# Optimization experiments

Measured on AMD Instinct MI355X. Metric: run time of the kernel, lower is better.

Reference implementation:

```python
import jax, jax.numpy as jnp
import numpy as np

NEG_SLOPE = 0.2


def gat_conv(h, src, dst, n_dst, W_src, W_dst, attn_l, attn_r, bias):
    # h: [N_src, F_in]; edges src->dst; dst nodes are a prefix of src nodes.
    H, D = attn_l.shape
    z_src = (h @ W_src).reshape(h.shape[0], H, D)          # [N_src, H, D]
    z_dst = (h[:n_dst] @ W_dst).reshape(n_dst, H, D)       # [N_dst, H, D]
    el = jnp.einsum('nhd,hd->nh', z_src, attn_l)           # [N_src, H]
    er = jnp.einsum('nhd,hd->nh', z_dst, attn_r)           # [N_dst, H]
    e = jax.nn.leaky_relu(el[src] + er[dst], NEG_SLOPE)    # [E, H]
    # numerically stable edge softmax over incoming edges of each dst node
    m = jax.ops.segment_max(e, dst, num_segments=n_dst)    # [N_dst, H]
    w = jnp.exp(e - m[dst])                                # [E, H]
    s = jax.ops.segment_sum(w, dst, num_segments=n_dst)    # [N_dst, H]
    alpha = w / s[dst]                                     # [E, H]
    msg = alpha[:, :, None] * z_src[src]                   # [E, H, D]
    out = jax.ops.segment_sum(msg, dst, num_segments=n_dst)
    return out + bias                                      # [N_dst, H, D]


def setup_inputs() -> dict:
    key = jax.random.key(0)
    ks = jax.random.split(key, 16)
    IN, HID, HEADS, NCLS = 256, 64, 4, 47
    N_SRC0, N_DST0, E0 = 200000, 50000, 500000
    N_DST1, E1 = 10000, 100000
    sc0 = 0.1
    inp = {
        'x': jax.random.normal(ks[0], (N_SRC0, IN), jnp.float32),
        'src0': jax.random.randint(ks[1], (E0,), 0, N_SRC0, jnp.int32),
        'dst0': jax.random.randint(ks[2], (E0,), 0, N_DST0, jnp.int32),
        'src1': jax.random.randint(ks[3], (E1,), 0, N_DST0, jnp.int32),
        'dst1': jax.random.randint(ks[4], (E1,), 0, N_DST1, jnp.int32),
        'num_dst0': N_DST0,
        'num_dst1': N_DST1,
        'W0_src': jax.random.normal(ks[5], (IN, HEADS * HID), jnp.float32) * sc0,
        'W0_dst': jax.random.normal(ks[6], (IN, HEADS * HID), jnp.float32) * sc0,
        'attn_l0': jax.random.normal(ks[7], (HEADS, HID), jnp.float32) * sc0,
        'attn_r0': jax.random.normal(ks[8], (HEADS, HID), jnp.float32) * sc0,
        'bias0': jnp.zeros((HEADS, HID), jnp.float32),
        'W1_src': jax.random.normal(ks[9], (HEADS * HID, HEADS * NCLS), jnp.float32) * sc0,
        'W1_dst': jax.random.normal(ks[10], (HEADS * HID, HEADS * NCLS), jnp.float32) * sc0,
        'attn_l1': jax.random.normal(ks[11], (HEADS, NCLS), jnp.float32) * sc0,
        'attn_r1': jax.random.normal(ks[12], (HEADS, NCLS), jnp.float32) * sc0,
        'bias1': jnp.zeros((HEADS, NCLS), jnp.float32),
    }
    return inp


def reference(x, src0, dst0, src1, dst1, num_dst0, num_dst1,
              W0_src, W0_dst, attn_l0, attn_r0, bias0,
              W1_src, W1_dst, attn_l1, attn_r1, bias1):
    # layer 0: GATConv + relu activation, flatten heads
    h = gat_conv(x, src0, dst0, num_dst0, W0_src, W0_dst, attn_l0, attn_r0, bias0)
    h = jax.nn.relu(h).reshape(num_dst0, -1)               # [N_dst0, H*HID]
    # layer 1: GATConv, no activation
    h = gat_conv(h, src1, dst1, num_dst1, W1_src, W1_dst, attn_l1, attn_r1, bias1)
    h = h.mean(axis=1)                                     # mean over heads -> [N_dst1, n_classes]
    return jax.nn.log_softmax(h, axis=-1)
```

## Files before the change

### kernel.cpp

```cpp
#include <hip/hip_runtime.h>
#include <math.h>

typedef _Float16 half8 __attribute__((ext_vector_type(8)));
typedef _Float16 half4 __attribute__((ext_vector_type(4)));
typedef float f32x16 __attribute__((ext_vector_type(16)));

constexpr int IN    = 256;
constexpr int NCLS  = 47;
constexpr int HD1   = 188;
constexpr float NEG_SLOPE = 0.2f;
constexpr int ND0 = 50000, ND1 = 10000;

static __device__ __forceinline__ float leaky(float x) {
    return x >= 0.f ? x : NEG_SLOPE * x;
}

__device__ __forceinline__ void gload16(const void* g, void* l) {
    __builtin_amdgcn_global_load_lds((const __attribute__((address_space(1))) void*)g,
                                     (__attribute__((address_space(3))) void*)l, 16, 0, 0);
}

__global__ __launch_bounds__(256) void prep_k(
        const float* __restrict__ W0s, const float* __restrict__ W1s,
        const float* __restrict__ W0d, const float* __restrict__ W1d,
        const float* __restrict__ ar0, const float* __restrict__ ar1,
        const float* __restrict__ b0,
        _Float16* __restrict__ B0t, _Float16* __restrict__ B1t,
        float* __restrict__ vr0T, float* __restrict__ vr1T, float* __restrict__ biasP) {
    int b = blockIdx.x, t = threadIdx.x;
    if (b < 256) {
        int id = b * 256 + t;
        int n = id >> 8, k = id & 255;
        B0t[n * 256 + k] = (_Float16)W0s[(size_t)k * 256 + n];
    } else if (b < 448) {
        int id = (b - 256) * 256 + t;
        int n = id >> 8, kpc = id & 255;
        int c = ((kpc & 7) << 5) | (kpc >> 3);
        B1t[n * 256 + kpc] = (n < HD1) ? (_Float16)W1s[(size_t)c * HD1 + n] : (_Float16)0.f;
    } else if (b == 448) {
        for (int i = t; i < 1024; i += 256) {
            int h = i >> 8, k = i & 255;
            float s = 0.f;
            for (int d = 0; d < 64; ++d) s += W0d[(size_t)k * 256 + h * 64 + d] * ar0[h * 64 + d];
            vr0T[h * 256 + k] = s;
        }
    } else if (b == 449) {
        for (int i = t; i < 1024; i += 256) {
            int h = i >> 8, kpc = i & 255;
            int c = ((kpc & 7) << 5) | (kpc >> 3);
            float s = 0.f;
            for (int d = 0; d < NCLS; ++d) s += W1d[(size_t)c * HD1 + h * NCLS + d] * ar1[h * NCLS + d];
            vr1T[h * 256 + kpc] = s;
        }
    } else {
        int c = ((t & 7) << 5) | (t >> 3);
        biasP[t] = b0[c];
    }
}

template <bool AHALF, int BCOLS, int NOUT, bool ZPC, int FEL>
__global__ __launch_bounds__(512, 2) void gemm32(const void* __restrict__ Av,
        const _Float16* __restrict__ Bt, void* __restrict__ Z,
        const float* __restrict__ attn_flat, float* __restrict__ el, int M, int ntiles) {
    constexpr int NCB  = BCOLS / 32;
    constexpr int ABUF = AHALF ? 1024 : 2048;
    __shared__ __align__(16) _Float16 Bs[BCOLS * 256];
    __shared__ __align__(16) char As[8 * 2 * ABUF];
    const int t = threadIdx.x, l = t & 63, w = t >> 6;
    const int l31 = l & 31, hi = l >> 5;
    const int G = gridDim.x;
    char* Areg = As + w * 2 * ABUF;

    constexpr int BITERS = (BCOLS * 32) / 512;
#pragma unroll
    for (int it = 0; it < BITERS; ++it) {
        int c = it * 512 + t;
        int col = c >> 5, sK = c & 31;
        int sKs = sK ^ (col & 7);
        gload16(Bt + (size_t)col * 256 + sKs * 8, (char*)Bs + (it * 512 + w * 64) * 16);
    }

    auto stageA = [&](int buf, int tile, int kst) {
        int base = tile * 256 + w * 32;
        if constexpr (AHALF) {
            int r = l >> 1, sl = l & 1;
            int row = base + r; if (row >= M) row = M - 1;
            int ks = sl ^ (r & 1);
            gload16((const _Float16*)Av + (size_t)row * 256 + kst * 16 + ks * 8,
                    Areg + buf * ABUF);
        } else {
#pragma unroll
            for (int i = 0; i < 2; ++i) {
                int c = i * 64 + l;
                int r = c >> 2, sl = c & 3;
                int row = base + r; if (row >= M) row = M - 1;
                int ks = sl ^ ((r >> 1) & 3);
                gload16((const float*)Av + (size_t)row * 256 + kst * 16 + ks * 4,
                        Areg + buf * ABUF + i * 1024);
            }
        }
    };

    int tile0 = blockIdx.x;
    stageA(0, tile0, 0);
    __syncthreads();

    float alv[NCB];
    int hs[NCB];
    if constexpr (FEL > 0) {
#pragma unroll
        for (int cb = 0; cb < NCB; ++cb) {
            int c = cb * 32 + l31;
            if constexpr (FEL == 1) { alv[cb] = attn_flat[c]; hs[cb] = cb >> 1; }
            else { alv[cb] = (c < NOUT) ? attn_flat[c] : 0.f;
                   hs[cb] = c < 47 ? 0 : c < 94 ? 1 : c < 141 ? 2 : 3; }
        }
    }

    int buf = 0;
    for (int tile = tile0; tile < ntiles; tile += G) {
        f32x16 acc[NCB];
#pragma unroll
        for (int cb = 0; cb < NCB; ++cb)
#pragma unroll
            for (int e = 0; e < 16; ++e) acc[cb][e] = 0.f;

#pragma unroll
        for (int kst = 0; kst < 16; ++kst) {
            if (kst < 15) {
                stageA(buf ^ 1, tile, kst + 1);
                if constexpr (AHALF) asm volatile("s_waitcnt vmcnt(1)" ::: "memory");
                else                 asm volatile("s_waitcnt vmcnt(2)" ::: "memory");
            } else if (tile + G < ntiles) {
                stageA(buf ^ 1, tile + G, 0);
                if constexpr (AHALF) asm volatile("s_waitcnt vmcnt(1)" ::: "memory");
                else                 asm volatile("s_waitcnt vmcnt(2)" ::: "memory");
            } else {
                asm volatile("s_waitcnt vmcnt(0)" ::: "memory");
            }
            half8 af;
            if constexpr (AHALF) {
                af = *(const half8*)(Areg + buf * ABUF + l31 * 32 + ((hi ^ (l31 & 1)) << 4));
            } else {
                const char* ab = Areg + buf * ABUF + l31 * 64;
                float4 f0 = *(const float4*)(ab + ((( 2 * hi)     ^ ((l31 >> 1) & 3)) << 4));
                float4 f1 = *(const float4*)(ab + (((2 * hi + 1) ^ ((l31 >> 1) & 3)) << 4));
                af[0] = (_Float16)f0.x; af[1] = (_Float16)f0.y;
                af[2] = (_Float16)f0.z; af[3] = (_Float16)f0.w;
                af[4] = (_Float16)f1.x; af[5] = (_Float16)f1.y;
                af[6] = (_Float16)f1.z; af[7] = (_Float16)f1.w;
            }
#pragma unroll
            for (int cb = 0; cb < NCB; ++cb) {
                half8 bf = *(const half8*)&Bs[(cb * 32 + l31) * 256 +
                                              (((kst * 2 + hi) ^ (l & 7)) << 3)];
                acc[cb] = __builtin_amdgcn_mfma_f32_32x32x16_f16(af, bf, acc[cb], 0, 0, 0);
            }
            buf ^= 1;
        }

        const int R0 = tile * 256 + w * 32;
#pragma unroll
        for (int q = 0; q < 16; ++q) {
            int row = (q & 3) + 8 * (q >> 2) + 4 * hi;
            int grow = R0 + row;
            if constexpr (ZPC) {
                half8 hv;
#pragma unroll
                for (int cb = 0; cb < NCB; ++cb) hv[cb] = (_Float16)acc[cb][q];
                if (grow < M)
                    *(half8*)((_Float16*)Z + (size_t)grow * 256 + l31 * 8) = hv;
            } else {
                if (grow < M) {
#pragma unroll
                    for (int cb = 0; cb < NCB; ++cb) {
                        int col = cb * 32 + l31;
                        if (col < NOUT)
                            ((float*)Z)[(size_t)grow * NOUT + col] = acc[cb][q];
                    }
                }
            }
            if constexpr (FEL > 0) {
                float sh0 = 0.f, sh1 = 0.f, sh2 = 0.f, sh3 = 0.f;
#pragma unroll
                for (int cb = 0; cb < NCB; ++cb) {
                    float v = acc[cb][q] * alv[cb];
                    sh0 += (hs[cb] == 0) ? v : 0.f;
                    sh1 += (hs[cb] == 1) ? v : 0.f;
                    sh2 += (hs[cb] == 2) ? v : 0.f;
                    sh3 += (hs[cb] == 3) ? v : 0.f;
                }
#pragma unroll
                for (int off = 1; off <= 16; off <<= 1) {
                    sh0 += __shfl_xor(sh0, off); sh1 += __shfl_xor(sh1, off);
                    sh2 += __shfl_xor(sh2, off); sh3 += __shfl_xor(sh3, off);
                }
                if (l31 == 0 && grow < M)
                    *(float4*)(el + (size_t)grow * 4) = make_float4(sh0, sh1, sh2, sh3);
            }
        }
    }
}

__global__ __launch_bounds__(256) void gemv_er_f32(const float* __restrict__ A,
        const float* __restrict__ vrT, float* __restrict__ er, int M) {
    int wv = threadIdx.x >> 6, lane = threadIdx.x & 63;
    int row = blockIdx.x * 4 + wv;
    if (row >= M) return;
    float4 xa = *(const float4*)(A + (size_t)row * IN + lane * 4);
    float s[4];
#pragma unroll
    for (int h = 0; h < 4; ++h) {
        float4 v = *(const float4*)(vrT + h * IN + lane * 4);
        s[h] = xa.x * v.x + xa.y * v.y + xa.z * v.z + xa.w * v.w;
    }
#pragma unroll
    for (int off = 32; off; off >>= 1)
#pragma unroll
        for (int h = 0; h < 4; ++h) s[h] += __shfl_xor(s[h], off);
    if (lane == 0) *(float4*)(er + (size_t)row * 4) = make_float4(s[0], s[1], s[2], s[3]);
}

__global__ __launch_bounds__(256) void gemv_er_f16(const _Float16* __restrict__ A,
        const float* __restrict__ vrT, float* __restrict__ er, int M) {
    int wv = threadIdx.x >> 6, lane = threadIdx.x & 63;
    int row = blockIdx.x * 4 + wv;
    if (row >= M) return;
    half4 ah = *(const half4*)(A + (size_t)row * IN + lane * 4);
    float a0 = (float)ah[0], a1 = (float)ah[1], a2 = (float)ah[2], a3 = (float)ah[3];
    float s[4];
#pragma unroll
    for (int h = 0; h < 4; ++h) {
        float4 v = *(const float4*)(vrT + h * IN + lane * 4);
        s[h] = a0 * v.x + a1 * v.y + a2 * v.z + a3 * v.w;
    }
#pragma unroll
    for (int off = 32; off; off >>= 1)
#pragma unroll
        for (int h = 0; h < 4; ++h) s[h] += __shfl_xor(s[h], off);
    if (lane == 0) *(float4*)(er + (size_t)row * 4) = make_float4(s[0], s[1], s[2], s[3]);
}

__global__ void hist2_k(const int* __restrict__ dst0, int E0,
                        const int* __restrict__ dst1, int E1, int* __restrict__ counts) {
    int i = blockIdx.x * blockDim.x + threadIdx.x;
    if (i < E0) atomicAdd(&counts[dst0[i]], 1);
    else if (i < E0 + E1) atomicAdd(&counts[ND0 + dst1[i - E0]], 1);
}

__global__ __launch_bounds__(256) void scan1_k(const int* __restrict__ counts, int n,
                                               int* __restrict__ part) {
    __shared__ int ws[4];
    int i = blockIdx.x * 256 + threadIdx.x;
    int lane = threadIdx.x & 63, wv = threadIdx.x >> 6;
    int s = (i < n) ? counts[i] : 0;
#pragma unroll
    for (int off = 32; off; off >>= 1) s += __shfl_xor(s, off);
    if (lane == 0) ws[wv] = s;
    __syncthreads();
    if (threadIdx.x == 0) part[blockIdx.x] = ws[0] + ws[1] + ws[2] + ws[3];
}

__global__ __launch_bounds__(256) void scan2_k(int* __restrict__ part, int nb) {
    __shared__ int ws[4];
    int tid = threadIdx.x, lane = tid & 63, wv = tid >> 6;
    int v = (tid < nb) ? part[tid] : 0;
    int x = v;
#pragma unroll
    for (int off = 1; off < 64; off <<= 1) {
        int u = __shfl_up(x, off);
        if (lane >= off) x += u;
    }
    if (lane == 63) ws[wv] = x;
    __syncthreads();
    int base = 0;
    for (int k = 0; k < wv; ++k) base += ws[k];
    if (tid < nb) part[tid] = base + x - v;
}

__global__ __launch_bounds__(256) void scan3_k(const int* __restrict__ counts, int n,
        const int* __restrict__ part, int* __restrict__ offsets, int* __restrict__ cursor) {
    __shared__ int ws[4];
    int i = blockIdx.x * 256 + threadIdx.x;
    int lane = threadIdx.x & 63, wv = threadIdx.x >> 6;
    int v = (i < n) ? counts[i] : 0;
    int x = v;
#pragma unroll
    for (int off = 1; off < 64; off <<= 1) {
        int u = __shfl_up(x, off);
        if (lane >= off) x += u;
    }
    if (lane == 63) ws[wv] = x;
    __syncthreads();
    int base = part[blockIdx.x];
    for (int k = 0; k < wv; ++k) base += ws[k];
    int off_ = base + x - v;
    if (i < n) { offsets[i] = off_; cursor[i] = off_; }
    if (i == n - 1) offsets[n] = off_ + v;
}

__global__ void scatter2_k(const int* __restrict__ src0, const int* __restrict__ dst0, int E0,
                           const int* __restrict__ src1, const int* __restrict__ dst1, int E1,
                           int* __restrict__ cursor, int* __restrict__ ssrc) {
    int i = blockIdx.x * blockDim.x + threadIdx.x;
    if (i < E0) {
        int p = atomicAdd(&cursor[dst0[i]], 1);
        ssrc[p] = src0[i];
    } else if (i < E0 + E1) {
        int j = i - E0;
        int p = atomicAdd(&cursor[ND0 + dst1[j]], 1);
        ssrc[p] = src1[j];
    }
}

__global__ __launch_bounds__(256) void agg_l0(const int* __restrict__ ssrc,
        const int* __restrict__ offs, const float* __restrict__ el,
        const float* __restrict__ er, const _Float16* __restrict__ z,
        const float* __restrict__ biasP, _Float16* __restrict__ h, int nd) {
    int wv = threadIdx.x >> 6, lane = threadIdx.x & 63;
    int d = blockIdx.x * 4 + wv;
    if (d >= nd) return;
    int beg = offs[d], end = offs[d + 1];
    float4 er4 = *(const float4*)(er + (size_t)d * 4);
    bool odd = lane & 1;
    float erlo = odd ? er4.z : er4.x;
    float erhi = odd ? er4.w : er4.y;
    float a0 = 0, a1 = 0, a2 = 0, a3 = 0, slo = 0, shi = 0;
    for (int j0 = beg; j0 < end; j0 += 64) {
        int nn = min(64, end - j0);
        int myidx = (lane < nn) ? ssrc[j0 + lane] : 0;
        int j = 0;
        for (; j + 4 <= nn; j += 4) {
            int s0 = __shfl(myidx, j),     s1 = __shfl(myidx, j + 1);
            int s2 = __shfl(myidx, j + 2), s3 = __shfl(myidx, j + 3);
            float4 e0 = *(const float4*)(el + (size_t)s0 * 4);
            float4 e1 = *(const float4*)(el + (size_t)s1 * 4);
            float4 e2 = *(const float4*)(el + (size_t)s2 * 4);
            float4 e3 = *(const float4*)(el + (size_t)s3 * 4);
            half4 z0v = *(const half4*)(z + (size_t)s0 * 256 + lane * 4);
            half4 z1v = *(const half4*)(z + (size_t)s1 * 256 + lane * 4);
            half4 z2v = *(const half4*)(z + (size_t)s2 * 256 + lane * 4);
            half4 z3v = *(const half4*)(z + (size_t)s3 * 256 + lane * 4);
            float wl0 = __expf(leaky((odd ? e0.z : e0.x) + erlo));
            float wh0 = __expf(leaky((odd ? e0.w : e0.y) + erhi));
            float wl1 = __expf(leaky((odd ? e1.z : e1.x) + erlo));
            float wh1 = __expf(leaky((odd ? e1.w : e1.y) + erhi));
            float wl2 = __expf(leaky((odd ? e2.z : e2.x) + erlo));
            float wh2 = __expf(leaky((odd ? e2.w : e2.y) + erhi));
            float wl3 = __expf(leaky((odd ? e3.z : e3.x) + erlo));
            float wh3 = __expf(leaky((odd ? e3.w : e3.y) + erhi));
            slo += (wl0 + wl1) + (wl2 + wl3);
            shi += (wh0 + wh1) + (wh2 + wh3);
            a0 += wl0 * (float)z0v[0] + wl1 * (float)z1v[0] + wl2 * (float)z2v[0] + wl3 * (float)z3v[0];
            a1 += wl0 * (float)z0v[1] + wl1 * (float)z1v[1] + wl2 * (float)z2v[1] + wl3 * (float)z3v[1];
            a2 += wh0 * (float)z0v[2] + wh1 * (float)z1v[2] + wh2 * (float)z2v[2] + wh3 * (float)z3v[2];
            a3 += wh0 * (float)z0v[3] + wh1 * (float)z1v[3] + wh2 * (float)z2v[3] + wh3 * (float)z3v[3];
        }
        for (; j < nn; ++j) {
            int s = __shfl(myidx, j);
            float4 e4 = *(const float4*)(el + (size_t)s * 4);
            half4 zv = *(const half4*)(z + (size_t)s * 256 + lane * 4);
            float wl = __expf(leaky((odd ? e4.z : e4.x) + erlo));
            float wh = __expf(leaky((odd ? e4.w : e4.y) + erhi));
            slo += wl; shi += wh;
            a0 += wl * (float)zv[0]; a1 += wl * (float)zv[1];
            a2 += wh * (float)zv[2]; a3 += wh * (float)zv[3];
        }
    }
    float ilo = slo > 0.f ? 1.f / slo : 0.f;
    float ihi = shi > 0.f ? 1.f / shi : 0.f;
    float4 b4 = *(const float4*)(biasP + lane * 4);
    half4 o;
    o[0] = (_Float16)fmaxf(a0 * ilo + b4.x, 0.f);
    o[1] = (_Float16)fmaxf(a1 * ilo + b4.y, 0.f);
    o[2] = (_Float16)fmaxf(a2 * ihi + b4.z, 0.f);
    o[3] = (_Float16)fmaxf(a3 * ihi + b4.w, 0.f);
    *(half4*)(h + (size_t)d * 256 + lane * 4) = o;
}

__global__ __launch_bounds__(256) void agg_l1f(const int* __restrict__ ssrc,
        const int* __restrict__ offs, const float* __restrict__ el,
        const float* __restrict__ er, const float* __restrict__ z,
        const float* __restrict__ bias, float* __restrict__ y, int nd) {
    __shared__ float ro[4][192];
    int wv = threadIdx.x >> 6, lane = threadIdx.x & 63;
    int d = blockIdx.x * 4 + wv;
    if (d >= nd) return;
    int beg = offs[ND0 + d], end = offs[ND0 + d + 1];
    float4 er4 = *(const float4*)(er + (size_t)d * 4);
    const int f0 = lane, f1 = lane + 64, f2 = lane + 128;
    const int h0 = f0 / NCLS, h1 = f1 / NCLS;
    const bool has2 = f2 < HD1;
    const int h2 = has2 ? f2 / NCLS : 3;
    float a0 = 0, a1 = 0, a2 = 0;
    float s0 = 0, s1 = 0, s2 = 0, s3 = 0;
    for (int j0 = beg; j0 < end; j0 += 64) {
        int nn = min(64, end - j0);
        int myidx = (lane < nn) ? ssrc[j0 + lane] : 0;
        int j = 0;
        for (; j + 2 <= nn; j += 2) {
            int sa_ = __shfl(myidx, j), sb_ = __shfl(myidx, j + 1);
            float4 ea = *(const float4*)(el + (size_t)sa_ * 4);
            float4 eb = *(const float4*)(el + (size_t)sb_ * 4);
            const float* za = z + (size_t)sa_ * HD1;
            const float* zb = z + (size_t)sb_ * HD1;
            float za0 = za[f0], za1 = za[f1], za2 = has2 ? za[f2] : 0.f;
            float zb0 = zb[f0], zb1 = zb[f1], zb2 = has2 ? zb[f2] : 0.f;
            float wa0 = __expf(leaky(ea.x + er4.x)), wa1 = __expf(leaky(ea.y + er4.y));
            float wa2 = __expf(leaky(ea.z + er4.z)), wa3 = __expf(leaky(ea.w + er4.w));
            float wb0 = __expf(leaky(eb.x + er4.x)), wb1 = __expf(leaky(eb.y + er4.y));
            float wb2 = __expf(leaky(eb.z + er4.z)), wb3 = __expf(leaky(eb.w + er4.w));
            s0 += wa0 + wb0; s1 += wa1 + wb1; s2 += wa2 + wb2; s3 += wa3 + wb3;
            a0 += (h0 == 0 ? wa0 : h0 == 1 ? wa1 : h0 == 2 ? wa2 : wa3) * za0
                + (h0 == 0 ? wb0 : h0 == 1 ? wb1 : h0 == 2 ? wb2 : wb3) * zb0;
            a1 += (h1 == 0 ? wa0 : h1 == 1 ? wa1 : h1 == 2 ? wa2 : wa3) * za1
                + (h1 == 0 ? wb0 : h1 == 1 ? wb1 : h1 == 2 ? wb2 : wb3) * zb1;
            if (has2)
                a2 += (h2 == 0 ? wa0 : h2 == 1 ? wa1 : h2 == 2 ? wa2 : wa3) * za2
                    + (h2 == 0 ? wb0 : h2 == 1 ? wb1 : h2 == 2 ? wb2 : wb3) * zb2;
        }
        for (; j < nn; ++j) {
            int s = __shfl(myidx, j);
            float4 e4 = *(const float4*)(el + (size_t)s * 4);
            float w0 = __expf(leaky(e4.x + er4.x));
            float w1 = __expf(leaky(e4.y + er4.y));
            float w2 = __expf(leaky(e4.z + er4.z));
            float w3 = __expf(leaky(e4.w + er4.w));
            s0 += w0; s1 += w1; s2 += w2; s3 += w3;
            const float* zr = z + (size_t)s * HD1;
            a0 += (h0 == 0 ? w0 : h0 == 1 ? w1 : h0 == 2 ? w2 : w3) * zr[f0];
            a1 += (h1 == 0 ? w0 : h1 == 1 ? w1 : h1 == 2 ? w2 : w3) * zr[f1];
            if (has2) a2 += (h2 == 0 ? w0 : h2 == 1 ? w1 : h2 == 2 ? w2 : w3) * zr[f2];
        }
    }
    float sa = h0 == 0 ? s0 : h0 == 1 ? s1 : h0 == 2 ? s2 : s3;
    float sb = h1 == 0 ? s0 : h1 == 1 ? s1 : h1 == 2 ? s2 : s3;
    float sc = h2 == 0 ? s0 : h2 == 1 ? s1 : h2 == 2 ? s2 : s3;
    ro[wv][f0] = a0 * (sa > 0.f ? 1.f / sa : 0.f) + bias[f0];
    ro[wv][f1] = a1 * (sb > 0.f ? 1.f / sb : 0.f) + bias[f1];
    if (has2) ro[wv][f2] = a2 * (sc > 0.f ? 1.f / sc : 0.f) + bias[f2];
    asm volatile("s_waitcnt lgkmcnt(0)" ::: "memory");
    __builtin_amdgcn_sched_barrier(0);
    float vv = 0.f, v = -INFINITY;
    if (lane < NCLS) {
        vv = 0.25f * (ro[wv][lane] + ro[wv][lane + NCLS] +
                      ro[wv][lane + 2 * NCLS] + ro[wv][lane + 3 * NCLS]);
        v = vv;
    }
    float mx = v;
#pragma unroll
    for (int off = 32; off; off >>= 1) mx = fmaxf(mx, __shfl_xor(mx, off));
    float pp = (lane < NCLS) ? __expf(vv - mx) : 0.f;
    float sum = pp;
#pragma unroll
    for (int off = 32; off; off >>= 1) sum += __shfl_xor(sum, off);
    if (lane < NCLS) y[(size_t)d * NCLS + lane] = vv - mx - logf(sum);
}

extern "C" void kernel_launch(void* const* d_in, const int* in_sizes, int n_in,
                              void* d_out, int out_size, void* d_ws, size_t ws_size,
                              hipStream_t stream) {
    const float* x    = (const float*)d_in[0];
    const int*   src0 = (const int*)d_in[1];
    const int*   dst0 = (const int*)d_in[2];
    const int*   src1 = (const int*)d_in[3];
    const int*   dst1 = (const int*)d_in[4];
    const float* W0s  = (const float*)d_in[7];
    const float* W0d  = (const float*)d_in[8];
    const float* al0  = (const float*)d_in[9];
    const float* ar0  = (const float*)d_in[10];
    const float* b0   = (const float*)d_in[11];
    const float* W1s  = (const float*)d_in[12];
    const float* W1d  = (const float*)d_in[13];
    const float* al1  = (const float*)d_in[14];
    const float* ar1  = (const float*)d_in[15];
    const float* b1   = (const float*)d_in[16];
    const int E0 = in_sizes[1], E1 = in_sizes[3];
    const int NS0 = in_sizes[0] / IN;

    char* p = (char*)d_ws;
    auto take = [&](size_t bytes) {
        char* r = p;
        p += (bytes + 255) & ~(size_t)255;
        return r;
    };
    _Float16* z0   = (_Float16*)take((size_t)NS0 * 256 * 2);
    _Float16* h    = (_Float16*)take((size_t)ND0 * 256 * 2);
    float*    z1   = (float*)take((size_t)ND0 * HD1 * 4);
    float*    el0  = (float*)take((size_t)NS0 * 4 * 4);
    float*    er0  = (float*)take((size_t)ND0 * 4 * 4);
    float*    el1  = (float*)take((size_t)ND0 * 4 * 4);
    float*    er1  = (float*)take((size_t)ND1 * 4 * 4);
    _Float16* B0t  = (_Float16*)take((size_t)256 * 256 * 2);
    _Float16* B1t  = (_Float16*)take((size_t)192 * 256 * 2);
    float*    vr0T = (float*)take(4 * 256 * 4);
    float*    vr1T = (float*)take(4 * 256 * 4);
    float*    biasP = (float*)take(256 * 4);
    const int NDT = ND0 + ND1;
    int* counts = (int*)take((size_t)NDT * 4);
    int* offs   = (int*)take((size_t)(NDT + 1) * 4);
    int* cur    = (int*)take((size_t)NDT * 4);
    int* ss     = (int*)take((size_t)(E0 + E1) * 4);
    int* part   = (int*)take(256 * 4);

    const int NB = (NDT + 255) / 256;
    const int NT0 = (NS0 + 255) / 256, NT1 = (ND0 + 255) / 256;
    const int G0 = NT0 < 256 ? NT0 : 256, G1 = NT1 < 256 ? NT1 : 256;

    hipMemsetAsync(counts, 0, (size_t)NDT * 4, stream);

    prep_k<<<451, 256, 0, stream>>>(W0s, W1s, W0d, W1d, ar0, ar1, b0,
                                    B0t, B1t, vr0T, vr1T, biasP);
    hist2_k<<<(E0 + E1 + 255) / 256, 256, 0, stream>>>(dst0, E0, dst1, E1, counts);
    scan1_k<<<NB, 256, 0, stream>>>(counts, NDT, part);
    scan2_k<<<1, 256, 0, stream>>>(part, NB);
    scan3_k<<<NB, 256, 0, stream>>>(counts, NDT, part, offs, cur);
    scatter2_k<<<(E0 + E1 + 255) / 256, 256, 0, stream>>>(src0, dst0, E0, src1, dst1, E1,
                                                          cur, ss);

    gemm32<false, 256, 256, true, 1><<<G0, 512, 0, stream>>>(
        (const void*)x, B0t, (void*)z0, al0, el0, NS0, NT0);
    gemv_er_f32<<<(ND0 + 3) / 4, 256, 0, stream>>>(x, vr0T, er0, ND0);
    agg_l0<<<(ND0 + 3) / 4, 256, 0, stream>>>(ss, offs, el0, er0, z0, biasP, h, ND0);

    gemm32<true, 192, 188, false, 2><<<G1, 512, 0, stream>>>(
        (const void*)h, B1t, (void*)z1, al1, el1, ND0, NT1);
    gemv_er_f16<<<(ND1 + 3) / 4, 256, 0, stream>>>(h, vr1T, er1, ND1);
    agg_l1f<<<(ND1 + 3) / 4, 256, 0, stream>>>(ss, offs, el1, er1, z1, b1,
                                               (float*)d_out, ND1);
}
```

Baseline: 302.4 us.

## Restructure projection GEMMs with register-resident weights and natural column layout

Replaces the 256-row-tile GEMM, which staged the whole weight matrix in LDS, with a kernel that keeps each wave's 32 weight columns in registers and streams 32-row tiles of activations through double-buffered LDS. This allows higher occupancy and a larger grid. The permuted column layout and the separate bias-permute pass are dropped. Layer-1 z is stored in fp16 to halve gather traffic, and layer-1 el is computed by a fused el/er GEMV rather than inside the GEMM epilogue. In exchange, each tile now waits on a full vmcnt(0) plus a barrier, and z1 loses precision.

```diff
diff --git a/kernel.cpp b/kernel.cpp
--- a/kernel.cpp
+++ b/kernel.cpp
@@ -23,10 +23,10 @@
 __global__ __launch_bounds__(256) void prep_k(
         const float* __restrict__ W0s, const float* __restrict__ W1s,
         const float* __restrict__ W0d, const float* __restrict__ W1d,
-        const float* __restrict__ ar0, const float* __restrict__ ar1,
-        const float* __restrict__ b0,
+        const float* __restrict__ ar0, const float* __restrict__ al1,
+        const float* __restrict__ ar1,
         _Float16* __restrict__ B0t, _Float16* __restrict__ B1t,
-        float* __restrict__ vr0T, float* __restrict__ vr1T, float* __restrict__ biasP) {
+        float* __restrict__ vr0T, float* __restrict__ vl1T, float* __restrict__ vr1T) {
     int b = blockIdx.x, t = threadIdx.x;
     if (b < 256) {
         int id = b * 256 + t;
@@ -34,171 +34,140 @@
         B0t[n * 256 + k] = (_Float16)W0s[(size_t)k * 256 + n];
     } else if (b < 448) {
         int id = (b - 256) * 256 + t;
-        int n = id >> 8, kpc = id & 255;
-        int c = ((kpc & 7) << 5) | (kpc >> 3);
-        B1t[n * 256 + kpc] = (n < HD1) ? (_Float16)W1s[(size_t)c * HD1 + n] : (_Float16)0.f;
+        int n = id >> 8, k = id & 255;
+        B1t[n * 256 + k] = (n < HD1) ? (_Float16)W1s[(size_t)k * HD1 + n] : (_Float16)0.f;
     } else if (b == 448) {
         for (int i = t; i < 1024; i += 256) {
             int h = i >> 8, k = i & 255;
             float s = 0.f;
-            for (int d = 0; d < 64; ++d) s += W0d[(size_t)k * 256 + h * 64 + d] * ar0[h * 64 + d];
+            for (int d = 0; d < 64; ++d)
+                s += W0d[(size_t)k * 256 + h * 64 + d] * ar0[h * 64 + d];
             vr0T[h * 256 + k] = s;
         }
     } else if (b == 449) {
         for (int i = t; i < 1024; i += 256) {
-            int h = i >> 8, kpc = i & 255;
-            int c = ((kpc & 7) << 5) | (kpc >> 3);
+            int h = i >> 8, k = i & 255;
             float s = 0.f;
-            for (int d = 0; d < NCLS; ++d) s += W1d[(size_t)c * HD1 + h * NCLS + d] * ar1[h * NCLS + d];
-            vr1T[h * 256 + kpc] = s;
+            for (int d = 0; d < NCLS; ++d)
+                s += W1s[(size_t)k * HD1 + h * NCLS + d] * al1[h * NCLS + d];
+            vl1T[h * 256 + k] = s;
         }
     } else {
-        int c = ((t & 7) << 5) | (t >> 3);
-        biasP[t] = b0[c];
-    }
-}
-
-template <bool AHALF, int BCOLS, int NOUT, bool ZPC, int FEL>
-__global__ __launch_bounds__(512, 2) void gemm32(const void* __restrict__ Av,
-        const _Float16* __restrict__ Bt, void* __restrict__ Z,
-        const float* __restrict__ attn_flat, float* __restrict__ el, int M, int ntiles) {
-    constexpr int NCB  = BCOLS / 32;
-    constexpr int ABUF = AHALF ? 1024 : 2048;
-    __shared__ __align__(16) _Float16 Bs[BCOLS * 256];
-    __shared__ __align__(16) char As[8 * 2 * ABUF];
+        for (int i = t; i < 1024; i += 256) {
+            int h = i >> 8, k = i & 255;
+            float s = 0.f;
+            for (int d = 0; d < NCLS; ++d)
+                s += W1d[(size_t)k * HD1 + h * NCLS + d] * ar1[h * NCLS + d];
+            vr1T[h * 256 + k] = s;
+        }
+    }
+}
+
+template <bool AHALF, int NWC, bool FEL>
+__global__ __launch_bounds__(512, 4) void gemmk(const void* __restrict__ Av,
+        const _Float16* __restrict__ Bt, _Float16* __restrict__ Z,
+        const float* __restrict__ al, float* __restrict__ el, int M, int ntiles) {
+    constexpr int ABYTES = AHALF ? 16 * 1040 : 32 * 1040;
+    __shared__ __align__(16) char As[2][ABYTES];
+    __shared__ float elp[2][8][32];
+    __shared__ float alds[256];
     const int t = threadIdx.x, l = t & 63, w = t >> 6;
     const int l31 = l & 31, hi = l >> 5;
     const int G = gridDim.x;
-    char* Areg = As + w * 2 * ABUF;
-
-    constexpr int BITERS = (BCOLS * 32) / 512;
-#pragma unroll
-    for (int it = 0; it < BITERS; ++it) {
-        int c = it * 512 + t;
-        int col = c >> 5, sK = c & 31;
-        int sKs = sK ^ (col & 7);
-        gload16(Bt + (size_t)col * 256 + sKs * 8, (char*)Bs + (it * 512 + w * 64) * 16);
-    }
-
-    auto stageA = [&](int buf, int tile, int kst) {
-        int base = tile * 256 + w * 32;
+
+    if (FEL && t < 256) alds[t] = al[t];
+
+    half8 wk[16];
+    {
+        int wc = (w < NWC) ? w * 32 + l31 : 0;
+        const _Float16* bp = Bt + (size_t)wc * 256 + hi * 8;
+#pragma unroll
+        for (int ks = 0; ks < 16; ++ks) wk[ks] = *(const half8*)(bp + ks * 16);
+    }
+
+    auto stage = [&](int buf, int tile) {
         if constexpr (AHALF) {
-            int r = l >> 1, sl = l & 1;
-            int row = base + r; if (row >= M) row = M - 1;
-            int ks = sl ^ (r & 1);
-            gload16((const _Float16*)Av + (size_t)row * 256 + kst * 16 + ks * 8,
-                    Areg + buf * ABUF);
+#pragma unroll
+            for (int i = 0; i < 2; ++i) {
+                int pr = w * 2 + i;
+                int row = tile * 32 + pr * 2 + hi;
+                if (row >= M) row = M - 1;
+                gload16((const _Float16*)Av + (size_t)row * 256 + l31 * 8,
+                        As[buf] + pr * 1040);
+            }
         } else {
 #pragma unroll
-            for (int i = 0; i < 2; ++i) {
-                int c = i * 64 + l;
-                int r = c >> 2, sl = c & 3;
-                int row = base + r; if (row >= M) row = M - 1;
-                int ks = sl ^ ((r >> 1) & 3);
-                gload16((const float*)Av + (size_t)row * 256 + kst * 16 + ks * 4,
-                        Areg + buf * ABUF + i * 1024);
+            for (int i = 0; i < 4; ++i) {
+                int r = w * 4 + i;
+                int row = tile * 32 + r;
+                if (row >= M) row = M - 1;
+                gload16((const float*)Av + (size_t)row * 256 + l * 4,
+                        As[buf] + r * 1040);
             }
         }
     };
 
     int tile0 = blockIdx.x;
-    stageA(0, tile0, 0);
+    stage(0, tile0);
+    asm volatile("s_waitcnt vmcnt(0)" ::: "memory");
     __syncthreads();
-
-    float alv[NCB];
-    int hs[NCB];
-    if constexpr (FEL > 0) {
-#pragma unroll
-        for (int cb = 0; cb < NCB; ++cb) {
-            int c = cb * 32 + l31;
-            if constexpr (FEL == 1) { alv[cb] = attn_flat[c]; hs[cb] = cb >> 1; }
-            else { alv[cb] = (c < NOUT) ? attn_flat[c] : 0.f;
-                   hs[cb] = c < 47 ? 0 : c < 94 ? 1 : c < 141 ? 2 : 3; }
-        }
-    }
 
     int buf = 0;
     for (int tile = tile0; tile < ntiles; tile += G) {
-        f32x16 acc[NCB];
-#pragma unroll
-        for (int cb = 0; cb < NCB; ++cb)
-#pragma unroll
-            for (int e = 0; e < 16; ++e) acc[cb][e] = 0.f;
-
-#pragma unroll
-        for (int kst = 0; kst < 16; ++kst) {
-            if (kst < 15) {
-                stageA(buf ^ 1, tile, kst + 1);
-                if constexpr (AHALF) asm volatile("s_waitcnt vmcnt(1)" ::: "memory");
-                else                 asm volatile("s_waitcnt vmcnt(2)" ::: "memory");
-            } else if (tile + G < ntiles) {
-                stageA(buf ^ 1, tile + G, 0);
-                if constexpr (AHALF) asm volatile("s_waitcnt vmcnt(1)" ::: "memory");
-                else                 asm volatile("s_waitcnt vmcnt(2)" ::: "memory");
-            } else {
-                asm volatile("s_waitcnt vmcnt(0)" ::: "memory");
-            }
-            half8 af;
-            if constexpr (AHALF) {
-                af = *(const half8*)(Areg + buf * ABUF + l31 * 32 + ((hi ^ (l31 & 1)) << 4));
-            } else {
-                const char* ab = Areg + buf * ABUF + l31 * 64;
-                float4 f0 = *(const float4*)(ab + ((( 2 * hi)     ^ ((l31 >> 1) & 3)) << 4));
-                float4 f1 = *(const float4*)(ab + (((2 * hi + 1) ^ ((l31 >> 1) & 3)) << 4));
-                af[0] = (_Float16)f0.x; af[1] = (_Float16)f0.y;
-                af[2] = (_Float16)f0.z; af[3] = (_Float16)f0.w;
-                af[4] = (_Float16)f1.x; af[5] = (_Float16)f1.y;
-                af[6] = (_Float16)f1.z; af[7] = (_Float16)f1.w;
-            }
-#pragma unroll
-            for (int cb = 0; cb < NCB; ++cb) {
-                half8 bf = *(const half8*)&Bs[(cb * 32 + l31) * 256 +
-                                              (((kst * 2 + hi) ^ (l & 7)) << 3)];
-                acc[cb] = __builtin_amdgcn_mfma_f32_32x32x16_f16(af, bf, acc[cb], 0, 0, 0);
-            }
-            buf ^= 1;
-        }
-
-        const int R0 = tile * 256 + w * 32;
-#pragma unroll
-        for (int q = 0; q < 16; ++q) {
-            int row = (q & 3) + 8 * (q >> 2) + 4 * hi;
-            int grow = R0 + row;
-            if constexpr (ZPC) {
-                half8 hv;
-#pragma unroll
-                for (int cb = 0; cb < NCB; ++cb) hv[cb] = (_Float16)acc[cb][q];
-                if (grow < M)
-                    *(half8*)((_Float16*)Z + (size_t)grow * 256 + l31 * 8) = hv;
-            } else {
-                if (grow < M) {
-#pragma unroll
-                    for (int cb = 0; cb < NCB; ++cb) {
-                        int col = cb * 32 + l31;
-                        if (col < NOUT)
-                            ((float*)Z)[(size_t)grow * NOUT + col] = acc[cb][q];
-                    }
+        int nxt = tile + G;
+        if (nxt < ntiles) stage(buf ^ 1, nxt);
+
+        if (w < NWC) {
+            f32x16 acc;
+#pragma unroll
+            for (int e = 0; e < 16; ++e) acc[e] = 0.f;
+#pragma unroll
+            for (int ks = 0; ks < 16; ++ks) {
+                half8 bf;
+                if constexpr (AHALF) {
+                    bf = *(const half8*)(As[buf] + (l31 >> 1) * 1040 + (l31 & 1) * 512
+                                         + ks * 32 + hi * 16);
+                } else {
+                    const char* ab = As[buf] + l31 * 1040 + ks * 64 + hi * 32;
+                    float4 f0 = *(const float4*)ab;
+                    float4 f1 = *(const float4*)(ab + 16);
+                    bf[0] = (_Float16)f0.x; bf[1] = (_Float16)f0.y;
+                    bf[2] = (_Float16)f0.z; bf[3] = (_Float16)f0.w;
+                    bf[4] = (_Float16)f1.x; bf[5] = (_Float16)f1.y;
+                    bf[6] = (_Float16)f1.z; bf[7] = (_Float16)f1.w;
                 }
-            }
-            if constexpr (FEL > 0) {
-                float sh0 = 0.f, sh1 = 0.f, sh2 = 0.f, sh3 = 0.f;
-#pragma unroll
-                for (int cb = 0; cb < NCB; ++cb) {
-                    float v = acc[cb][q] * alv[cb];
-                    sh0 += (hs[cb] == 0) ? v : 0.f;
-                    sh1 += (hs[cb] == 1) ? v : 0.f;
-                    sh2 += (hs[cb] == 2) ? v : 0.f;
-                    sh3 += (hs[cb] == 3) ? v : 0.f;
+                acc = __builtin_amdgcn_mfma_f32_32x32x16_f16(wk[ks], bf, acc, 0, 0, 0);
+            }
+            int xrow = tile * 32 + l31;
+            if (xrow < M) {
+#pragma unroll
+                for (int g = 0; g < 4; ++g) {
+                    half4 hv;
+                    hv[0] = (_Float16)acc[g * 4 + 0]; hv[1] = (_Float16)acc[g * 4 + 1];
+                    hv[2] = (_Float16)acc[g * 4 + 2]; hv[3] = (_Float16)acc[g * 4 + 3];
+                    *(half4*)(Z + (size_t)xrow * (NWC * 32) + w * 32 + g * 8 + hi * 4) = hv;
                 }
-#pragma unroll
-                for (int off = 1; off <= 16; off <<= 1) {
-                    sh0 += __shfl_xor(sh0, off); sh1 += __shfl_xor(sh1, off);
-                    sh2 += __shfl_xor(sh2, off); sh3 += __shfl_xor(sh3, off);
-                }
-                if (l31 == 0 && grow < M)
-                    *(float4*)(el + (size_t)grow * 4) = make_float4(sh0, sh1, sh2, sh3);
-            }
-        }
+            }
+            if constexpr (FEL) {
+                float s = 0.f;
+#pragma unroll
+                for (int q = 0; q < 16; ++q)
+                    s += acc[q] * alds[w * 32 + (q & 3) + 8 * (q >> 2) + 4 * hi];
+                s += __shfl_xor(s, 32);
+                if (hi == 0) elp[buf][w][l31] = s;
+            }
+        }
+        asm volatile("s_waitcnt vmcnt(0)" ::: "memory");
+        __syncthreads();
+        if constexpr (FEL) {
+            if (w < 4 && hi == 0) {
+                int xrow = tile * 32 + l31;
+                if (xrow < M)
+                    el[(size_t)xrow * 4 + w] =
+                        elp[buf][2 * w][l31] + elp[buf][2 * w + 1][l31];
+            }
+        }
+        buf ^= 1;
     }
 }
 
@@ -221,24 +190,34 @@
     if (lane == 0) *(float4*)(er + (size_t)row * 4) = make_float4(s[0], s[1], s[2], s[3]);
 }
 
-__global__ __launch_bounds__(256) void gemv_er_f16(const _Float16* __restrict__ A,
-        const float* __restrict__ vrT, float* __restrict__ er, int M) {
+__global__ __launch_bounds__(256) void gemv_lr_f16(const _Float16* __restrict__ A,
+        const float* __restrict__ vlT, const float* __restrict__ vrT,
+        float* __restrict__ el, float* __restrict__ er, int M, int Mr) {
     int wv = threadIdx.x >> 6, lane = threadIdx.x & 63;
     int row = blockIdx.x * 4 + wv;
     if (row >= M) return;
     half4 ah = *(const half4*)(A + (size_t)row * IN + lane * 4);
     float a0 = (float)ah[0], a1 = (float)ah[1], a2 = (float)ah[2], a3 = (float)ah[3];
-    float s[4];
+    float sl[4], sr[4];
 #pragma unroll
     for (int h = 0; h < 4; ++h) {
-        float4 v = *(const float4*)(vrT + h * IN + lane * 4);
-        s[h] = a0 * v.x + a1 * v.y + a2 * v.z + a3 * v.w;
+        float4 v = *(const float4*)(vlT + h * IN + lane * 4);
+        sl[h] = a0 * v.x + a1 * v.y + a2 * v.z + a3 * v.w;
+        float4 u = *(const float4*)(vrT + h * IN + lane * 4);
+        sr[h] = a0 * u.x + a1 * u.y + a2 * u.z + a3 * u.w;
     }
 #pragma unroll
     for (int off = 32; off; off >>= 1)
 #pragma unroll
-        for (int h = 0; h < 4; ++h) s[h] += __shfl_xor(s[h], off);
-    if (lane == 0) *(float4*)(er + (size_t)row * 4) = make_float4(s[0], s[1], s[2], s[3]);
+        for (int h = 0; h < 4; ++h) {
+            sl[h] += __shfl_xor(sl[h], off);
+            sr[h] += __shfl_xor(sr[h], off);
+        }
+    if (lane == 0) {
+        *(float4*)(el + (size_t)row * 4) = make_float4(sl[0], sl[1], sl[2], sl[3]);
+        if (row < Mr)
+            *(float4*)(er + (size_t)row * 4) = make_float4(sr[0], sr[1], sr[2], sr[3]);
+    }
 }
 
 __global__ void hist2_k(const int* __restrict__ dst0, int E0,
@@ -316,16 +295,14 @@
 __global__ __launch_bounds__(256) void agg_l0(const int* __restrict__ ssrc,
         const int* __restrict__ offs, const float* __restrict__ el,
         const float* __restrict__ er, const _Float16* __restrict__ z,
-        const float* __restrict__ biasP, _Float16* __restrict__ h, int nd) {
+        const float* __restrict__ bias, _Float16* __restrict__ h, int nd) {
     int wv = threadIdx.x >> 6, lane = threadIdx.x & 63;
     int d = blockIdx.x * 4 + wv;
     if (d >= nd) return;
+    int head = lane >> 4;
     int beg = offs[d], end = offs[d + 1];
-    float4 er4 = *(const float4*)(er + (size_t)d * 4);
-    bool odd = lane & 1;
-    float erlo = odd ? er4.z : er4.x;
-    float erhi = odd ? er4.w : er4.y;
-    float a0 = 0, a1 = 0, a2 = 0, a3 = 0, slo = 0, shi = 0;
+    float erh = er[(size_t)d * 4 + head];
+    float ax = 0, ay = 0, az = 0, aw = 0, ssum = 0;
     for (int j0 = beg; j0 < end; j0 += 64) {
         int nn = min(64, end - j0);
         int myidx = (lane < nn) ? ssrc[j0 + lane] : 0;
@@ -333,54 +310,43 @@
         for (; j + 4 <= nn; j += 4) {
             int s0 = __shfl(myidx, j),     s1 = __shfl(myidx, j + 1);
             int s2 = __shfl(myidx, j + 2), s3 = __shfl(myidx, j + 3);
-            float4 e0 = *(const float4*)(el + (size_t)s0 * 4);
-            float4 e1 = *(const float4*)(el + (size_t)s1 * 4);
-            float4 e2 = *(const float4*)(el + (size_t)s2 * 4);
-            float4 e3 = *(const float4*)(el + (size_t)s3 * 4);
-            half4 z0v = *(const half4*)(z + (size_t)s0 * 256 + lane * 4);
-            half4 z1v = *(const half4*)(z + (size_t)s1 * 256 + lane * 4);
-            half4 z2v = *(const half4*)(z + (size_t)s2 * 256 + lane * 4);
-            half4 z3v = *(const half4*)(z + (size_t)s3 * 256 + lane * 4);
-            float wl0 = __expf(leaky((odd ? e0.z : e0.x) + erlo));
-            float wh0 = __expf(leaky((odd ? e0.w : e0.y) + erhi));
-            float wl1 = __expf(leaky((odd ? e1.z : e1.x) + erlo));
-            float wh1 = __expf(leaky((odd ? e1.w : e1.y) + erhi));
-            float wl2 = __expf(leaky((odd ? e2.z : e2.x) + erlo));
-            float wh2 = __expf(leaky((odd ? e2.w : e2.y) + erhi));
-            float wl3 = __expf(leaky((odd ? e3.z : e3.x) + erlo));
-            float wh3 = __expf(leaky((odd ? e3.w : e3.y) + erhi));
-            slo += (wl0 + wl1) + (wl2 + wl3);
-            shi += (wh0 + wh1) + (wh2 + wh3);
-            a0 += wl0 * (float)z0v[0] + wl1 * (float)z1v[0] + wl2 * (float)z2v[0] + wl3 * (float)z3v[0];
-            a1 += wl0 * (float)z0v[1] + wl1 * (float)z1v[1] + wl2 * (float)z2v[1] + wl3 * (float)z3v[1];
-            a2 += wh0 * (float)z0v[2] + wh1 * (float)z1v[2] + wh2 * (float)z2v[2] + wh3 * (float)z3v[2];
-            a3 += wh0 * (float)z0v[3] + wh1 * (float)z1v[3] + wh2 * (float)z2v[3] + wh3 * (float)z3v[3];
+            float e0 = el[(size_t)s0 * 4 + head], e1 = el[(size_t)s1 * 4 + head];
+            float e2 = el[(size_t)s2 * 4 + head], e3 = el[(size_t)s3 * 4 + head];
+            half4 zv0 = *(const half4*)(z + (size_t)s0 * 256 + lane * 4);
+            half4 zv1 = *(const half4*)(z + (size_t)s1 * 256 + lane * 4);
+            half4 zv2 = *(const half4*)(z + (size_t)s2 * 256 + lane * 4);
+            half4 zv3 = *(const half4*)(z + (size_t)s3 * 256 + lane * 4);
+            float w0 = __expf(leaky(e0 + erh)), w1 = __expf(leaky(e1 + erh));
+            float w2 = __expf(leaky(e2 + erh)), w3 = __expf(leaky(e3 + erh));
+            ssum += (w0 + w1) + (w2 + w3);
+            ax += w0 * (float)zv0[0] + w1 * (float)zv1[0] + w2 * (float)zv2[0] + w3 * (float)zv3[0];
+            ay += w0 * (float)zv0[1] + w1 * (float)zv1[1] + w2 * (float)zv2[1] + w3 * (float)zv3[1];
+            az += w0 * (float)zv0[2] + w1 * (float)zv1[2] + w2 * (float)zv2[2] + w3 * (float)zv3[2];
+            aw += w0 * (float)zv0[3] + w1 * (float)zv1[3] + w2 * (float)zv2[3] + w3 * (float)zv3[3];
         }
         for (; j < nn; ++j) {
             int s = __shfl(myidx, j);
-            float4 e4 = *(const float4*)(el + (size_t)s * 4);
+            float e = el[(size_t)s * 4 + head] + erh;
+            float wgt = __expf(leaky(e));
+            ssum += wgt;
             half4 zv = *(const half4*)(z + (size_t)s * 256 + lane * 4);
-            float wl = __expf(leaky((odd ? e4.z : e4.x) + erlo));
-            float wh = __expf(leaky((odd ? e4.w : e4.y) + erhi));
-            slo += wl; shi += wh;
-            a0 += wl * (float)zv[0]; a1 += wl * (float)zv[1];
-            a2 += wh * (float)zv[2]; a3 += wh * (float)zv[3];
-        }
-    }
-    float ilo = slo > 0.f ? 1.f / slo : 0.f;
-    float ihi = shi > 0.f ? 1.f / shi : 0.f;
-    float4 b4 = *(const float4*)(biasP + lane * 4);
+            ax += wgt * (float)zv[0]; ay += wgt * (float)zv[1];
+            az += wgt * (float)zv[2]; aw += wgt * (float)zv[3];
+        }
+    }
+    float inv = ssum > 0.f ? 1.f / ssum : 0.f;
+    const float* b = bias + lane * 4;
     half4 o;
-    o[0] = (_Float16)fmaxf(a0 * ilo + b4.x, 0.f);
-    o[1] = (_Float16)fmaxf(a1 * ilo + b4.y, 0.f);
-    o[2] = (_Float16)fmaxf(a2 * ihi + b4.z, 0.f);
-    o[3] = (_Float16)fmaxf(a3 * ihi + b4.w, 0.f);
+    o[0] = (_Float16)fmaxf(ax * inv + b[0], 0.f);
+    o[1] = (_Float16)fmaxf(ay * inv + b[1], 0.f);
+    o[2] = (_Float16)fmaxf(az * inv + b[2], 0.f);
+    o[3] = (_Float16)fmaxf(aw * inv + b[3], 0.f);
     *(half4*)(h + (size_t)d * 256 + lane * 4) = o;
 }
 
 __global__ __launch_bounds__(256) void agg_l1f(const int* __restrict__ ssrc,
         const int* __restrict__ offs, const float* __restrict__ el,
-        const float* __restrict__ er, const float* __restrict__ z,
+        const float* __restrict__ er, const _Float16* __restrict__ z,
         const float* __restrict__ bias, float* __restrict__ y, int nd) {
     __shared__ float ro[4][192];
     int wv = threadIdx.x >> 6, lane = threadIdx.x & 63;
@@ -402,10 +368,10 @@
             int sa_ = __shfl(myidx, j), sb_ = __shfl(myidx, j + 1);
             float4 ea = *(const float4*)(el + (size_t)sa_ * 4);
             float4 eb = *(const float4*)(el + (size_t)sb_ * 4);
-            const float* za = z + (size_t)sa_ * HD1;
-            const float* zb = z + (size_t)sb_ * HD1;
-            float za0 = za[f0], za1 = za[f1], za2 = has2 ? za[f2] : 0.f;
-            float zb0 = zb[f0], zb1 = zb[f1], zb2 = has2 ? zb[f2] : 0.f;
+            const _Float16* za = z + (size_t)sa_ * 192;
+            const _Float16* zb = z + (size_t)sb_ * 192;
+            float za0 = (float)za[f0], za1 = (float)za[f1], za2 = has2 ? (float)za[f2] : 0.f;
+            float zb0 = (float)zb[f0], zb1 = (float)zb[f1], zb2 = has2 ? (float)zb[f2] : 0.f;
             float wa0 = __expf(leaky(ea.x + er4.x)), wa1 = __expf(leaky(ea.y + er4.y));
             float wa2 = __expf(leaky(ea.z + er4.z)), wa3 = __expf(leaky(ea.w + er4.w));
             float wb0 = __expf(leaky(eb.x + er4.x)), wb1 = __expf(leaky(eb.y + er4.y));
@@ -427,10 +393,10 @@
             float w2 = __expf(leaky(e4.z + er4.z));
             float w3 = __expf(leaky(e4.w + er4.w));
             s0 += w0; s1 += w1; s2 += w2; s3 += w3;
-            const float* zr = z + (size_t)s * HD1;
-            a0 += (h0 == 0 ? w0 : h0 == 1 ? w1 : h0 == 2 ? w2 : w3) * zr[f0];
-            a1 += (h1 == 0 ? w0 : h1 == 1 ? w1 : h1 == 2 ? w2 : w3) * zr[f1];
-            if (has2) a2 += (h2 == 0 ? w0 : h2 == 1 ? w1 : h2 == 2 ? w2 : w3) * zr[f2];
+            const _Float16* zr = z + (size_t)s * 192;
+            a0 += (h0 == 0 ? w0 : h0 == 1 ? w1 : h0 == 2 ? w2 : w3) * (float)zr[f0];
+            a1 += (h1 == 0 ? w0 : h1 == 1 ? w1 : h1 == 2 ? w2 : w3) * (float)zr[f1];
+            if (has2) a2 += (h2 == 0 ? w0 : h2 == 1 ? w1 : h2 == 2 ? w2 : w3) * (float)zr[f2];
         }
     }
     float sa = h0 == 0 ? s0 : h0 == 1 ? s1 : h0 == 2 ? s2 : s3;
@@ -486,7 +452,7 @@
     };
     _Float16* z0   = (_Float16*)take((size_t)NS0 * 256 * 2);
     _Float16* h    = (_Float16*)take((size_t)ND0 * 256 * 2);
-    float*    z1   = (float*)take((size_t)ND0 * HD1 * 4);
+    _Float16* z1   = (_Float16*)take((size_t)ND0 * 192 * 2);
     float*    el0  = (float*)take((size_t)NS0 * 4 * 4);
     float*    er0  = (float*)take((size_t)ND0 * 4 * 4);
     float*    el1  = (float*)take((size_t)ND0 * 4 * 4);
@@ -494,8 +460,8 @@
     _Float16* B0t  = (_Float16*)take((size_t)256 * 256 * 2);
     _Float16* B1t  = (_Float16*)take((size_t)192 * 256 * 2);
     float*    vr0T = (float*)take(4 * 256 * 4);
+    float*    vl1T = (float*)take(4 * 256 * 4);
     float*    vr1T = (float*)take(4 * 256 * 4);
-    float*    biasP = (float*)take(256 * 4);
     const int NDT = ND0 + ND1;
     int* counts = (int*)take((size_t)NDT * 4);
     int* offs   = (int*)take((size_t)(NDT + 1) * 4);
@@ -504,13 +470,13 @@
     int* part   = (int*)take(256 * 4);
 
     const int NB = (NDT + 255) / 256;
-    const int NT0 = (NS0 + 255) / 256, NT1 = (ND0 + 255) / 256;
-    const int G0 = NT0 < 256 ? NT0 : 256, G1 = NT1 < 256 ? NT1 : 256;
+    const int NT0 = (NS0 + 31) / 32, NT1 = (ND0 + 31) / 32;
+    const int G0 = NT0 < 512 ? NT0 : 512, G1 = NT1 < 512 ? NT1 : 512;
 
     hipMemsetAsync(counts, 0, (size_t)NDT * 4, stream);
 
-    prep_k<<<451, 256, 0, stream>>>(W0s, W1s, W0d, W1d, ar0, ar1, b0,
-                                    B0t, B1t, vr0T, vr1T, biasP);
+    prep_k<<<451, 256, 0, stream>>>(W0s, W1s, W0d, W1d, ar0, al1, ar1,
+                                    B0t, B1t, vr0T, vl1T, vr1T);
     hist2_k<<<(E0 + E1 + 255) / 256, 256, 0, stream>>>(dst0, E0, dst1, E1, counts);
     scan1_k<<<NB, 256, 0, stream>>>(counts, NDT, part);
     scan2_k<<<1, 256, 0, stream>>>(part, NB);
@@ -518,14 +484,14 @@
     scatter2_k<<<(E0 + E1 + 255) / 256, 256, 0, stream>>>(src0, dst0, E0, src1, dst1, E1,
                                                           cur, ss);
 
-    gemm32<false, 256, 256, true, 1><<<G0, 512, 0, stream>>>(
-        (const void*)x, B0t, (void*)z0, al0, el0, NS0, NT0);
+    gemmk<false, 8, true><<<G0, 512, 0, stream>>>(
+        (const void*)x, B0t, z0, al0, el0, NS0, NT0);
     gemv_er_f32<<<(ND0 + 3) / 4, 256, 0, stream>>>(x, vr0T, er0, ND0);
-    agg_l0<<<(ND0 + 3) / 4, 256, 0, stream>>>(ss, offs, el0, er0, z0, biasP, h, ND0);
-
-    gemm32<true, 192, 188, false, 2><<<G1, 512, 0, stream>>>(
-        (const void*)h, B1t, (void*)z1, al1, el1, ND0, NT1);
-    gemv_er_f16<<<(ND1 + 3) / 4, 256, 0, stream>>>(h, vr1T, er1, ND1);
+    agg_l0<<<(ND0 + 3) / 4, 256, 0, stream>>>(ss, offs, el0, er0, z0, b0, h, ND0);
+
+    gemmk<true, 6, false><<<G1, 512, 0, stream>>>(
+        (const void*)h, B1t, z1, nullptr, nullptr, ND0, NT1);
+    gemv_lr_f16<<<(ND0 + 3) / 4, 256, 0, stream>>>(h, vl1T, vr1T, el1, er1, ND0, ND1);
     agg_l1f<<<(ND1 + 3) / 4, 256, 0, stream>>>(ss, offs, el1, er1, z1, b1,
                                                (float*)d_out, ND1);
 }
```

After: 321.9 us. 6.4% more time.
